# Optimization experiments

Hardware: AMD Instinct MI355X
Metric: run time of the kernel (lower is better)

The kernel has to match this reference:

```python
import jax, jax.numpy as jnp
import numpy as np

B, T, NX = 4, 6, 128
F_IN, H, F_OUT = 64, 128, 64
N = T * NX * NX  # 98304 cubed-sphere nodes


def _build_neighbors():
    # 4-neighbor grid adjacency per tile (periodic within tile), [N, 4] int32.
    t = np.arange(T)[:, None, None]
    i = np.arange(NX)[None, :, None]
    j = np.arange(NX)[None, None, :]

    def nid(tt, ii, jj):
        return tt * NX * NX + (ii % NX) * NX + (jj % NX)

    nbr = np.stack(
        [nid(t, i - 1, j), nid(t, i + 1, j), nid(t, i, j - 1), nid(t, i, j + 1)],
        axis=-1,
    ).reshape(-1, 4)
    return jnp.asarray(nbr, dtype=jnp.int32)


def setup_inputs() -> dict:
    key = jax.random.key(0)
    ks = jax.random.split(key, 20)
    inp = {
        "inputs": jax.random.normal(ks[0], (B, T, NX, NX, F_IN), dtype=jnp.float32),
        "nbr": _build_neighbors(),
    }
    # SAGEConv channel chain: 64->128, 128->64, 64->32, 32->32, 64->64, 128->64
    dims = [(F_IN, H), (H, H // 2), (H // 2, H // 4), (H // 4, H // 4), (H // 2, H // 2), (H, F_OUT)]
    k = 1
    for li, (din, dout) in enumerate(dims, start=1):
        s = 1.0 / np.sqrt(din)
        inp[f"W_self_{li}"] = jax.random.normal(ks[k], (din, dout), dtype=jnp.float32) * s
        inp[f"W_neigh_{li}"] = jax.random.normal(ks[k + 1], (din, dout), dtype=jnp.float32) * s
        inp[f"b_{li}"] = jnp.zeros((dout,), dtype=jnp.float32)
        k += 2
    return inp


def _sage(h, nbr, Ws, Wn, b):
    # h: [N, B, F]. Mean over the 4 fixed grid neighbors, then self+neighbor linear.
    m = (h[nbr[:, 0]] + h[nbr[:, 1]] + h[nbr[:, 2]] + h[nbr[:, 3]]) * 0.25
    return h @ Ws + m @ Wn + b


def reference(inputs, nbr,
              W_self_1, W_neigh_1, b_1, W_self_2, W_neigh_2, b_2,
              W_self_3, W_neigh_3, b_3, W_self_4, W_neigh_4, b_4,
              W_self_5, W_neigh_5, b_5, W_self_6, W_neigh_6, b_6):
    b, t, nx, ny, f = inputs.shape
    x = inputs.reshape(b, t * nx * ny, f).transpose(1, 0, 2)  # [N, B, F]
    act = jax.nn.relu
    # num_blocks = 1
    h1 = act(_sage(x, nbr, W_self_1, W_neigh_1, b_1))
    h2 = act(_sage(h1, nbr, W_self_2, W_neigh_2, b_2))
    h3 = act(_sage(h2, nbr, W_self_3, W_neigh_3, b_3))
    h4 = act(_sage(h3, nbr, W_self_4, W_neigh_4, b_4))
    h5 = jnp.concatenate([act(_sage(h4, nbr, W_self_4, W_neigh_4, b_4)), h3], axis=-1)
    h6 = jnp.concatenate([act(_sage(h5, nbr, W_self_5, W_neigh_5, b_5)), h2], axis=-1)
    out = _sage(h6, nbr, W_self_6, W_neigh_6, b_6)  # [N, B, F_OUT]
    return out.transpose(1, 0, 2).reshape(b, t, nx, ny, -1)
```

## Files before the change

kernel.cpp:

```cpp
#include <hip/hip_runtime.h>
#include <type_traits>

#define NNODES 98304
#define NB 4
#define NX 128
#define FACE (NX * NX)

typedef __attribute__((ext_vector_type(8))) short short8;
typedef __attribute__((ext_vector_type(8))) unsigned short ushort8;
typedef __attribute__((ext_vector_type(4))) float f32x4;

__device__ __forceinline__ float bf2f(unsigned short u) {
  union { unsigned int u; float f; } c; c.u = ((unsigned int)u) << 16; return c.f;
}
__device__ __forceinline__ unsigned short f2bf(float f) {
  union { float f; unsigned int u; } c; c.f = f;
  unsigned int r = 0x7FFFu + ((c.u >> 16) & 1u);
  return (unsigned short)((c.u + r) >> 16);
}
__device__ __forceinline__ unsigned int cvtpk(float lo, float hi) {
  unsigned int r;
  asm("v_cvt_pk_bf16_f32 %0, %1, %2" : "=v"(r) : "v"(lo), "v"(hi));
  return r;
}

__device__ __forceinline__ int4 nbr4(int n) {
  const int base = n & ~(FACE - 1);
  const int i = (n >> 7) & (NX - 1);
  const int j = n & (NX - 1);
  const int iu = (i + NX - 1) & (NX - 1), id = (i + 1) & (NX - 1);
  const int jl = (j + NX - 1) & (NX - 1), jr = (j + 1) & (NX - 1);
  return make_int4(base + (iu << 7) + j, base + (id << 7) + j,
                   base + (i << 7) + jl, base + (i << 7) + jr);
}

__device__ __forceinline__ void tile_barrier() {
  asm volatile("s_waitcnt lgkmcnt(0)" ::: "memory");
  __builtin_amdgcn_s_barrier();
  asm volatile("" ::: "memory");
}

constexpr int rows_for(int FIN)            { return FIN == 32 ? 64 : 32; }
constexpr int grid_for(int FIN, int SRCK)  { return (FIN == 128 || SRCK == 0) ? 1024 : 1536; }
constexpr int minw_for(int FIN, int SRCK)  { return (FIN == 128 || SRCK == 0) ? 4 : 6; }

template<int FIN, int FOUT, int SRCK, int DSTK, bool RELU>
__global__ __launch_bounds__(256, minw_for(FIN, SRCK))
void sage_mfma(const void* __restrict__ srcp, int sstride, int soff,
               void* __restrict__ dstp, int dstride, int doff,
               const float* __restrict__ Ws, const float* __restrict__ Wn,
               const float* __restrict__ bias)
{
  constexpr int ROWS = rows_for(FIN);
  constexpr int GRID = grid_for(FIN, SRCK);
  constexpr int NPT = ROWS / 4;
  constexpr int NTILES = (NNODES * NB) / ROWS;
  constexpr int K = 2 * FIN;
  constexpr int KSTEPS = K / 32;
  constexpr int LD = K + 8;
  constexpr int WAVES_N = (FOUT >= 64) ? 4 : 2;
  constexpr int WAVES_M = 4 / WAVES_N;
  constexpr int CF = FOUT / (16 * WAVES_N);
  constexpr int RF = ROWS / (16 * WAVES_M);
  constexpr int CHUNKS = FIN / 8;
  constexpr int ITERS = (ROWS * CHUNKS) / 256;
  constexpr int PF = ITERS;

  __shared__ unsigned short As[2][ROWS][LD];

  const int tid = threadIdx.x;
  const int wave = tid >> 6, lane = tid & 63;
  const int wn = wave % WAVES_N, wm = wave / WAVES_N;
  const int colbase = wn * (FOUT / WAVES_N);
  const int rowbase = wm * (ROWS / WAVES_M);
  const int fn = lane & 15, fg = lane >> 4;

  short8 Bfrag[KSTEPS][CF];
  float bv[CF];
  #pragma unroll
  for (int ks = 0; ks < KSTEPS; ++ks) {
    const float* wb = (ks * 32 < FIN) ? (Ws + (size_t)(ks * 32) * FOUT)
                                      : (Wn + (size_t)(ks * 32 - FIN) * FOUT);
    #pragma unroll
    for (int cf = 0; cf < CF; ++cf) {
      const int col = colbase + cf * 16 + fn;
      short8 f;
      #pragma unroll
      for (int j = 0; j < 8; ++j)
        f[j] = (short)f2bf(wb[(size_t)(fg * 8 + j) * FOUT + col]);
      Bfrag[ks][cf] = f;
    }
  }
  #pragma unroll
  for (int cf = 0; cf < CF; ++cf) bv[cf] = bias[colbase + cf * 16 + fn];

  struct G0 { float4 s0, s1, a0, a1, b0, b1, c0, c1, d0, d1; };
  struct G1 { ushort8 s, n0, n1, n2, n3; };
  using PG = typename std::conditional<SRCK == 0, G0, G1>::type;

  auto issue = [&](int node0, int it, PG& p) {
    const int g = tid + it * 256;
    const int r = g / CHUNKS;
    const int c = (g - r * CHUNKS) * 8;
    const int n = node0 + (r >> 2);
    const int b = r & 3;
    const int4 nb4 = nbr4(n);
    if constexpr (SRCK == 0) {
      const float* s = (const float*)srcp;
      const float* ps = s + ((size_t)b * NNODES + n) * FIN + c;
      const float* p0 = s + ((size_t)b * NNODES + nb4.x) * FIN + c;
      const float* p1 = s + ((size_t)b * NNODES + nb4.y) * FIN + c;
      const float* p2 = s + ((size_t)b * NNODES + nb4.z) * FIN + c;
      const float* p3 = s + ((size_t)b * NNODES + nb4.w) * FIN + c;
      p.s0 = *(const float4*)ps; p.s1 = *(const float4*)(ps + 4);
      p.a0 = *(const float4*)p0; p.a1 = *(const float4*)(p0 + 4);
      p.b0 = *(const float4*)p1; p.b1 = *(const float4*)(p1 + 4);
      p.c0 = *(const float4*)p2; p.c1 = *(const float4*)(p2 + 4);
      p.d0 = *(const float4*)p3; p.d1 = *(const float4*)(p3 + 4);
    } else {
      const unsigned short* s = (const unsigned short*)srcp;
      auto ld = [&](int nn) {
        return *reinterpret_cast<const ushort8*>(s + ((size_t)nn * NB + b) * sstride + soff + c);
      };
      p.s = ld(n); p.n0 = ld(nb4.x); p.n1 = ld(nb4.y); p.n2 = ld(nb4.z); p.n3 = ld(nb4.w);
    }
  };

  auto finish = [&](int buf, int it, PG& p) {
    const int g = tid + it * 256;
    const int r = g / CHUNKS;
    const int c = (g - r * CHUNKS) * 8;
    uint4 xv, mv;
    if constexpr (SRCK == 0) {
      xv = make_uint4(cvtpk(p.s0.x, p.s0.y), cvtpk(p.s0.z, p.s0.w),
                      cvtpk(p.s1.x, p.s1.y), cvtpk(p.s1.z, p.s1.w));
      float4 m0, m1;
      m0.x = (p.a0.x + p.b0.x) + (p.c0.x + p.d0.x);
      m0.y = (p.a0.y + p.b0.y) + (p.c0.y + p.d0.y);
      m0.z = (p.a0.z + p.b0.z) + (p.c0.z + p.d0.z);
      m0.w = (p.a0.w + p.b0.w) + (p.c0.w + p.d0.w);
      m1.x = (p.a1.x + p.b1.x) + (p.c1.x + p.d1.x);
      m1.y = (p.a1.y + p.b1.y) + (p.c1.y + p.d1.y);
      m1.z = (p.a1.z + p.b1.z) + (p.c1.z + p.d1.z);
      m1.w = (p.a1.w + p.b1.w) + (p.c1.w + p.d1.w);
      mv = make_uint4(cvtpk(m0.x * 0.25f, m0.y * 0.25f), cvtpk(m0.z * 0.25f, m0.w * 0.25f),
                      cvtpk(m1.x * 0.25f, m1.y * 0.25f), cvtpk(m1.z * 0.25f, m1.w * 0.25f));
    } else {
      union { ushort8 s; uint4 u; } pun;
      pun.s = p.s;
      xv = pun.u;
      float sum[8];
      #pragma unroll
      for (int j = 0; j < 8; ++j)
        sum[j] = (bf2f(p.n0[j]) + bf2f(p.n1[j])) + (bf2f(p.n2[j]) + bf2f(p.n3[j]));
      mv = make_uint4(cvtpk(sum[0] * 0.25f, sum[1] * 0.25f), cvtpk(sum[2] * 0.25f, sum[3] * 0.25f),
                      cvtpk(sum[4] * 0.25f, sum[5] * 0.25f), cvtpk(sum[6] * 0.25f, sum[7] * 0.25f));
    }
    *reinterpret_cast<uint4*>(&As[buf][r][c]) = xv;
    *reinterpret_cast<uint4*>(&As[buf][r][FIN + c]) = mv;
  };

  {
    PG p[ITERS];
    #pragma unroll
    for (int it = 0; it < ITERS; ++it) issue(blockIdx.x * NPT, it, p[it]);
    #pragma unroll
    for (int it = 0; it < ITERS; ++it) finish(0, it, p[it]);
  }

  int cur = 0;
  for (int tile = blockIdx.x; tile < NTILES; tile += GRID) {
    const int node0 = tile * NPT;
    const bool hasnext = (tile + GRID) < NTILES;
    const int nnode0 = (tile + GRID) * NPT;

    PG ptop[PF];
    if (hasnext) {
      #pragma unroll
      for (int it = 0; it < PF; ++it) issue(nnode0, it, ptop[it]);
    }

    tile_barrier();

    f32x4 acc[RF][CF];
    #pragma unroll
    for (int rf = 0; rf < RF; ++rf)
      #pragma unroll
      for (int cf = 0; cf < CF; ++cf)
        acc[rf][cf] = (f32x4){bv[cf], bv[cf], bv[cf], bv[cf]};

    #pragma unroll
    for (int ks = 0; ks < KSTEPS; ++ks) {
      short8 a[RF];
      #pragma unroll
      for (int rf = 0; rf < RF; ++rf)
        a[rf] = *reinterpret_cast<const short8*>(&As[cur][rowbase + rf * 16 + fn][ks * 32 + fg * 8]);
      #pragma unroll
      for (int rf = 0; rf < RF; ++rf)
        #pragma unroll
        for (int cf = 0; cf < CF; ++cf)
          acc[rf][cf] = __builtin_amdgcn_mfma_f32_16x16x32_bf16(
              a[rf], Bfrag[ks][cf], acc[rf][cf], 0, 0, 0);
    }

    #pragma unroll
    for (int rf = 0; rf < RF; ++rf) {
      #pragma unroll
      for (int cf = 0; cf < CF; ++cf) {
        const int col = colbase + cf * 16 + fn;
        #pragma unroll
        for (int j = 0; j < 4; ++j) {
          const int row = rowbase + rf * 16 + fg * 4 + j;
          const int n = node0 + (row >> 2);
          const int b = row & 3;
          float v = acc[rf][cf][j];
          if (RELU) v = fmaxf(v, 0.f);
          if (DSTK == 0)
            ((float*)dstp)[((size_t)b * NNODES + n) * FOUT + col] = v;
          else
            ((unsigned short*)dstp)[((size_t)n * NB + b) * dstride + doff + col] = f2bf(v);
        }
      }
    }

    if (hasnext) {
      #pragma unroll
      for (int it = 0; it < PF; ++it) finish(cur ^ 1, it, ptop[it]);
    }
    cur ^= 1;
  }
}

extern "C" void kernel_launch(void* const* d_in, const int* in_sizes, int n_in,
                              void* d_out, int out_size, void* d_ws, size_t ws_size,
                              hipStream_t stream) {
  const float* x  = (const float*)d_in[0];
  const float* W1s = (const float*)d_in[2],  *W1n = (const float*)d_in[3],  *b1 = (const float*)d_in[4];
  const float* W2s = (const float*)d_in[5],  *W2n = (const float*)d_in[6],  *b2 = (const float*)d_in[7];
  const float* W3s = (const float*)d_in[8],  *W3n = (const float*)d_in[9],  *b3 = (const float*)d_in[10];
  const float* W4s = (const float*)d_in[11], *W4n = (const float*)d_in[12], *b4 = (const float*)d_in[13];
  const float* W5s = (const float*)d_in[14], *W5n = (const float*)d_in[15], *b5 = (const float*)d_in[16];
  const float* W6s = (const float*)d_in[17], *W6n = (const float*)d_in[18], *b6 = (const float*)d_in[19];

  unsigned short* h1 = (unsigned short*)d_out;
  unsigned short* h6 = (unsigned short*)d_ws;
  unsigned short* h5 = (unsigned short*)d_out;
  unsigned short* h4 = (unsigned short*)((char*)d_out + (size_t)NNODES * NB * 64 * 2);

  const dim3 block(256);

  sage_mfma<64, 128, 0, 1, true><<<dim3(grid_for(64, 0)), block, 0, stream>>>(x, 0, 0, h1, 128, 0, W1s, W1n, b1);
  sage_mfma<128, 64, 1, 1, true><<<dim3(grid_for(128, 1)), block, 0, stream>>>(h1, 128, 0, h6, 128, 64, W2s, W2n, b2);
  sage_mfma<64, 32, 1, 1, true><<<dim3(grid_for(64, 1)), block, 0, stream>>>(h6, 128, 64, h5, 64, 32, W3s, W3n, b3);
  sage_mfma<32, 32, 1, 1, true><<<dim3(grid_for(32, 1)), block, 0, stream>>>(h5, 64, 32, h4, 32, 0, W4s, W4n, b4);
  sage_mfma<32, 32, 1, 1, true><<<dim3(grid_for(32, 1)), block, 0, stream>>>(h4, 32, 0, h5, 64, 0, W4s, W4n, b4);
  sage_mfma<64, 64, 1, 1, true><<<dim3(grid_for(64, 1)), block, 0, stream>>>(h5, 64, 0, h6, 128, 0, W5s, W5n, b5);
  sage_mfma<128, 64, 1, 0, false><<<dim3(grid_for(128, 1)), block, 0, stream>>>(h6, 128, 0, d_out, 0, 0, W6s, W6n, b6);
}
```

Measured before the change: 219.6 us.

## Deepen gather prefetch to two tiles ahead with paired-tile loop

Restructures the persistent tile loop to process tiles in pairs with two register prefetch sets, so global gathers for a tile are issued two iterations before they are consumed. The aim is to hide more gather latency behind the MFMA compute. It also fixes the grid at 1024 blocks for every layer and lowers the occupancy hint in launch bounds, giving more registers per thread for the extra prefetch state at the cost of fewer resident waves. The new loop assumes the tile count divides evenly into pairs per block.

```diff
diff --git a/kernel.cpp b/kernel.cpp
--- a/kernel.cpp
+++ b/kernel.cpp
@@ -41,8 +41,8 @@
 }
 
 constexpr int rows_for(int FIN)            { return FIN == 32 ? 64 : 32; }
-constexpr int grid_for(int FIN, int SRCK)  { return (FIN == 128 || SRCK == 0) ? 1024 : 1536; }
-constexpr int minw_for(int FIN, int SRCK)  { return (FIN == 128 || SRCK == 0) ? 4 : 6; }
+constexpr int grid_for(int FIN, int SRCK)  { return 1024; }
+constexpr int minw_for(int FIN, int SRCK)  { return (FIN == 128 || SRCK == 0) ? 3 : 4; }
 
 template<int FIN, int FOUT, int SRCK, int DSTK, bool RELU>
 __global__ __launch_bounds__(256, minw_for(FIN, SRCK))
@@ -55,6 +55,7 @@
   constexpr int GRID = grid_for(FIN, SRCK);
   constexpr int NPT = ROWS / 4;
   constexpr int NTILES = (NNODES * NB) / ROWS;
+  constexpr int NPAIR = NTILES / GRID / 2;
   constexpr int K = 2 * FIN;
   constexpr int KSTEPS = K / 32;
   constexpr int LD = K + 8;
@@ -64,7 +65,6 @@
   constexpr int RF = ROWS / (16 * WAVES_M);
   constexpr int CHUNKS = FIN / 8;
   constexpr int ITERS = (ROWS * CHUNKS) / 256;
-  constexpr int PF = ITERS;
 
   __shared__ unsigned short As[2][ROWS][LD];
 
@@ -160,41 +160,19 @@
     *reinterpret_cast<uint4*>(&As[buf][r][FIN + c]) = mv;
   };
 
-  {
-    PG p[ITERS];
-    #pragma unroll
-    for (int it = 0; it < ITERS; ++it) issue(blockIdx.x * NPT, it, p[it]);
-    #pragma unroll
-    for (int it = 0; it < ITERS; ++it) finish(0, it, p[it]);
-  }
-
-  int cur = 0;
-  for (int tile = blockIdx.x; tile < NTILES; tile += GRID) {
-    const int node0 = tile * NPT;
-    const bool hasnext = (tile + GRID) < NTILES;
-    const int nnode0 = (tile + GRID) * NPT;
-
-    PG ptop[PF];
-    if (hasnext) {
-      #pragma unroll
-      for (int it = 0; it < PF; ++it) issue(nnode0, it, ptop[it]);
-    }
-
-    tile_barrier();
-
+  auto compute_store = [&](int buf, int node0) {
     f32x4 acc[RF][CF];
     #pragma unroll
     for (int rf = 0; rf < RF; ++rf)
       #pragma unroll
       for (int cf = 0; cf < CF; ++cf)
         acc[rf][cf] = (f32x4){bv[cf], bv[cf], bv[cf], bv[cf]};
-
     #pragma unroll
     for (int ks = 0; ks < KSTEPS; ++ks) {
       short8 a[RF];
       #pragma unroll
       for (int rf = 0; rf < RF; ++rf)
-        a[rf] = *reinterpret_cast<const short8*>(&As[cur][rowbase + rf * 16 + fn][ks * 32 + fg * 8]);
+        a[rf] = *reinterpret_cast<const short8*>(&As[buf][rowbase + rf * 16 + fn][ks * 32 + fg * 8]);
       #pragma unroll
       for (int rf = 0; rf < RF; ++rf)
         #pragma unroll
@@ -202,7 +180,6 @@
           acc[rf][cf] = __builtin_amdgcn_mfma_f32_16x16x32_bf16(
               a[rf], Bfrag[ks][cf], acc[rf][cf], 0, 0, 0);
     }
-
     #pragma unroll
     for (int rf = 0; rf < RF; ++rf) {
       #pragma unroll
@@ -222,12 +199,44 @@
         }
       }
     }
-
-    if (hasnext) {
-      #pragma unroll
-      for (int it = 0; it < PF; ++it) finish(cur ^ 1, it, ptop[it]);
-    }
-    cur ^= 1;
+  };
+
+  const int bid = blockIdx.x;
+
+  PG pA[ITERS], pB[ITERS];
+  {
+    PG p0[ITERS];
+    #pragma unroll
+    for (int it = 0; it < ITERS; ++it) issue(bid * NPT, it, p0[it]);
+    #pragma unroll
+    for (int it = 0; it < ITERS; ++it) finish(0, it, p0[it]);
+  }
+  #pragma unroll
+  for (int it = 0; it < ITERS; ++it) issue((bid + GRID) * NPT, it, pA[it]);
+
+  for (int k = 0; k < NPAIR; ++k) {
+    const int t0 = bid + 2 * k * GRID;
+    const bool last = (k == NPAIR - 1);
+
+    if (!last) {
+      #pragma unroll
+      for (int it = 0; it < ITERS; ++it) issue((t0 + 2 * GRID) * NPT, it, pB[it]);
+    }
+    tile_barrier();
+    compute_store(0, t0 * NPT);
+    #pragma unroll
+    for (int it = 0; it < ITERS; ++it) finish(1, it, pA[it]);
+
+    if (!last) {
+      #pragma unroll
+      for (int it = 0; it < ITERS; ++it) issue((t0 + 3 * GRID) * NPT, it, pA[it]);
+    }
+    tile_barrier();
+    compute_store(1, (t0 + GRID) * NPT);
+    if (!last) {
+      #pragma unroll
+      for (int it = 0; it < ITERS; ++it) finish(0, it, pB[it]);
+    }
   }
 }
 
```

New measurement: 227.8 us. +3.7%, slower.
